# Kernel tuning notes

Hardware: AMD Instinct MI355X
Metric: run time of the kernel (lower is better)

Reference implementation:

```python
import jax, jax.numpy as jnp
import numpy as np

ALPHA = 0.25
GAMMA = 2.0
EPS = 1e-8
W_CLASS = 2.0
W_BBOX = 5.0
W_GIOU = 2.0
B, Q, T, C = 64, 900, 300, 80


def setup_inputs() -> dict:
    key = jax.random.key(0)
    k1, k2, k3, k4 = jax.random.split(key, 4)
    pred_logits = jax.random.normal(k1, (B, Q, C), dtype=jnp.float32)
    pred_boxes = jax.random.uniform(k2, (B, Q, 4), dtype=jnp.float32)  # cxcywh in (0,1)
    tgt_labels = jax.random.randint(k3, (B, T), 0, C, dtype=jnp.int64)
    tgt_boxes = jax.random.uniform(k4, (B, T, 4), dtype=jnp.float32)
    return {"pred_logits": pred_logits, "pred_boxes": pred_boxes,
            "tgt_labels": tgt_labels, "tgt_boxes": tgt_boxes}


def box_cxcywh_to_xyxy(b):
    cx, cy, w, h = b[..., 0], b[..., 1], b[..., 2], b[..., 3]
    return jnp.stack([cx - 0.5 * w, cy - 0.5 * h, cx + 0.5 * w, cy + 0.5 * h], axis=-1)


def pairwise_giou(boxes1, boxes2):
    # boxes1: [B,Q,4] xyxy, boxes2: [B,T,4] xyxy -> [B,Q,T]
    area1 = (boxes1[..., 2] - boxes1[..., 0]) * (boxes1[..., 3] - boxes1[..., 1])
    area2 = (boxes2[..., 2] - boxes2[..., 0]) * (boxes2[..., 3] - boxes2[..., 1])
    lt = jnp.maximum(boxes1[:, :, None, :2], boxes2[:, None, :, :2])
    rb = jnp.minimum(boxes1[:, :, None, 2:], boxes2[:, None, :, 2:])
    wh = jnp.clip(rb - lt, 0.0)
    inter = wh[..., 0] * wh[..., 1]
    union = area1[:, :, None] + area2[:, None, :] - inter
    iou = inter / union
    lt_c = jnp.minimum(boxes1[:, :, None, :2], boxes2[:, None, :, :2])
    rb_c = jnp.maximum(boxes1[:, :, None, 2:], boxes2[:, None, :, 2:])
    wh_c = jnp.clip(rb_c - lt_c, 0.0)
    area_c = wh_c[..., 0] * wh_c[..., 1]
    return iou - (area_c - union) / area_c


def reference(pred_logits, pred_boxes, tgt_labels, tgt_boxes):
    # Batched cost matrix of HungarianMatcher (use_focal_loss=True).
    prob = jax.nn.sigmoid(pred_logits)  # [B,Q,C]
    idx = jnp.broadcast_to(tgt_labels[:, None, :], (prob.shape[0], prob.shape[1], tgt_labels.shape[1]))
    p = jnp.take_along_axis(prob, idx.astype(jnp.int32), axis=2)  # [B,Q,T]
    neg_cost = (1.0 - ALPHA) * p ** GAMMA * (-jnp.log(1.0 - p + EPS))
    pos_cost = ALPHA * (1.0 - p) ** GAMMA * (-jnp.log(p + EPS))
    cost_class = pos_cost - neg_cost
    cost_bbox = jnp.abs(pred_boxes[:, :, None, :] - tgt_boxes[:, None, :, :]).sum(-1)
    cost_giou = -pairwise_giou(box_cxcywh_to_xyxy(pred_boxes), box_cxcywh_to_xyxy(tgt_boxes))
    cost = W_BBOX * cost_bbox + W_CLASS * cost_class + W_GIOU * cost_giou
    return jnp.nan_to_num(cost, nan=1.0, posinf=1e6, neginf=-1e6)
```

## Files before the change

kernel.cpp:

```cpp
#include <hip/hip_runtime.h>


constexpr int B = 64, Q = 900, T = 300, C = 80;
constexpr int QTILE = 25;
constexpr int BLOCK = 320;
constexpr float ALPHA = 0.25f;
constexpr float EPSF  = 1e-8f;

__device__ __forceinline__ float fast_rcp(float x) {
    return __builtin_amdgcn_rcpf(x);
}

__global__ __launch_bounds__(BLOCK) void matcher_cost_kernel(
    const float* __restrict__ logits,
    const float* __restrict__ pboxes,
    const int*   __restrict__ tlabels,
    const float* __restrict__ tboxes,
    float* __restrict__ out)
{
    __shared__ float  s_cls[QTILE * C];
    __shared__ float4 s_pA[QTILE];
    __shared__ float4 s_pB[QTILE];

    const int bid = blockIdx.x;
    const int b   = bid / (Q / QTILE);
    const int q0  = (bid % (Q / QTILE)) * QTILE;
    const int tid = threadIdx.x;

    float tcx = 0.f, tcy = 0.f, tw = 0.f, th = 0.f;
    float tx0 = 0.f, ty0 = 0.f, tx1 = 0.f, ty1 = 0.f, ta = 0.f;
    int lab = 0;
    if (tid < T) {
        float4 bx = *(const float4*)(tboxes + ((size_t)b * T + tid) * 4);
        tcx = bx.x; tcy = bx.y; tw = bx.z; th = bx.w;
        tx0 = bx.x - 0.5f * bx.z; ty0 = bx.y - 0.5f * bx.w;
        tx1 = bx.x + 0.5f * bx.z; ty1 = bx.y + 0.5f * bx.w;
        ta  = bx.z * bx.w;
        lab = tlabels[(size_t)b * T + tid];
    }

    if (tid < QTILE) {
        float4 bx = *(const float4*)(pboxes + ((size_t)b * Q + q0 + tid) * 4);
        float x0 = bx.x - 0.5f * bx.z, y0 = bx.y - 0.5f * bx.w;
        float x1 = bx.x + 0.5f * bx.z, y1 = bx.y + 0.5f * bx.w;
        s_pA[tid] = bx;
        s_pB[tid] = make_float4(x0, y0, x1, y1);
    }

    {
        const float* lg = logits + ((size_t)b * Q + q0) * C;
        for (int i = tid; i < QTILE * C; i += BLOCK) {
            float x  = lg[i];
            float pr = fast_rcp(1.0f + __expf(-x));
            float om = 1.0f - pr;
            float pos = ALPHA * om * om * (-__logf(pr + EPSF));
            float neg = (1.0f - ALPHA) * pr * pr * (-__logf(om + EPSF));
            s_cls[i] = 2.0f * (pos - neg) + 2.0f;
        }
    }

    __syncthreads();

    if (tid >= T) return;

    const float* clscol = s_cls + lab;
    float* op = out + ((size_t)b * Q + q0) * T + tid;
    #pragma unroll 5
    for (int ql = 0; ql < QTILE; ++ql) {
        float4 pA = s_pA[ql];
        float4 pB = s_pB[ql];
        float  pa = pA.z * pA.w;
        float clsv = clscol[ql * C];

        float cbbox = fabsf(pA.x - tcx) + fabsf(pA.y - tcy) +
                      fabsf(pA.z - tw ) + fabsf(pA.w - th );

        float iw = fmaxf(fminf(pB.z, tx1) - fmaxf(pB.x, tx0), 0.0f);
        float ih = fmaxf(fminf(pB.w, ty1) - fmaxf(pB.y, ty0), 0.0f);
        float inter = iw * ih;
        float uni   = pa + ta - inter;

        float cw = fmaxf(pB.z, tx1) - fminf(pB.x, tx0);
        float ch = fmaxf(pB.w, ty1) - fminf(pB.y, ty0);
        float ca = cw * ch;

        float c = fmaf(5.0f, cbbox, clsv);
        c = fmaf(-2.0f * inter, fast_rcp(uni), c);
        c = fmaf(-2.0f * uni,   fast_rcp(ca),  c);

        if (c != c) c = 1.0f;

        op[(size_t)ql * T] = c;
    }
}

extern "C" void kernel_launch(void* const* d_in, const int* in_sizes, int n_in,
                              void* d_out, int out_size, void* d_ws, size_t ws_size,
                              hipStream_t stream) {
    const float* logits  = (const float*)d_in[0];
    const float* pboxes  = (const float*)d_in[1];
    const int*   tlabels = (const int*)  d_in[2];
    const float* tboxes  = (const float*)d_in[3];
    float* out = (float*)d_out;

    dim3 grid(B * (Q / QTILE));
    dim3 block(BLOCK);
    matcher_cost_kernel<<<grid, block, 0, stream>>>(logits, pboxes, tlabels, tboxes, out);
}
```

Measured before the change: 38.21 us.

## Shrink Q tile, read pred boxes directly from global, preload class costs

Reduces the Q tile from 25 to 20 so the logits loop divides evenly by the block size and can be fully unrolled. Prediction boxes are no longer staged in shared memory. Each thread now loads them as uniform float4s from global memory and recomputes the xyxy corners itself. The per-thread class costs are gathered from shared memory into a register array up front, and the main loop is fully unrolled. This trades shared-memory staging and a sync dependency for more registers, redundant corner math, and more blocks with less work each.

Measured after the change: 37.28 us. -2.4%, faster.

```diff
diff --git a/kernel.cpp b/kernel.cpp
--- a/kernel.cpp
+++ b/kernel.cpp
@@ -2,7 +2,7 @@
 
 
 constexpr int B = 64, Q = 900, T = 300, C = 80;
-constexpr int QTILE = 25;
+constexpr int QTILE = 20;
 constexpr int BLOCK = 320;
 constexpr float ALPHA = 0.25f;
 constexpr float EPSF  = 1e-8f;
@@ -18,9 +18,7 @@
     const float* __restrict__ tboxes,
     float* __restrict__ out)
 {
-    __shared__ float  s_cls[QTILE * C];
-    __shared__ float4 s_pA[QTILE];
-    __shared__ float4 s_pB[QTILE];
+    __shared__ float s_cls[QTILE * C];
 
     const int bid = blockIdx.x;
     const int b   = bid / (Q / QTILE);
@@ -39,17 +37,11 @@
         lab = tlabels[(size_t)b * T + tid];
     }
 
-    if (tid < QTILE) {
-        float4 bx = *(const float4*)(pboxes + ((size_t)b * Q + q0 + tid) * 4);
-        float x0 = bx.x - 0.5f * bx.z, y0 = bx.y - 0.5f * bx.w;
-        float x1 = bx.x + 0.5f * bx.z, y1 = bx.y + 0.5f * bx.w;
-        s_pA[tid] = bx;
-        s_pB[tid] = make_float4(x0, y0, x1, y1);
-    }
-
     {
         const float* lg = logits + ((size_t)b * Q + q0) * C;
-        for (int i = tid; i < QTILE * C; i += BLOCK) {
+        #pragma unroll
+        for (int s = 0; s < QTILE * C / BLOCK; ++s) {
+            int i = s * BLOCK + tid;
             float x  = lg[i];
             float pr = fast_rcp(1.0f + __expf(-x));
             float om = 1.0f - pr;
@@ -63,28 +55,37 @@
 
     if (tid >= T) return;
 
-    const float* clscol = s_cls + lab;
+    float clsr[QTILE];
+    {
+        const float* cp = s_cls + lab;
+        #pragma unroll
+        for (int ql = 0; ql < QTILE; ++ql)
+            clsr[ql] = cp[ql * C];
+    }
+
+    const float4* pb = (const float4*)(pboxes + ((size_t)b * Q + q0) * 4);
     float* op = out + ((size_t)b * Q + q0) * T + tid;
-    #pragma unroll 5
+
+    #pragma unroll
     for (int ql = 0; ql < QTILE; ++ql) {
-        float4 pA = s_pA[ql];
-        float4 pB = s_pB[ql];
-        float  pa = pA.z * pA.w;
-        float clsv = clscol[ql * C];
+        float4 pA = pb[ql];
+        float px0 = pA.x - 0.5f * pA.z, py0 = pA.y - 0.5f * pA.w;
+        float px1 = pA.x + 0.5f * pA.z, py1 = pA.y + 0.5f * pA.w;
+        float pa  = pA.z * pA.w;
 
         float cbbox = fabsf(pA.x - tcx) + fabsf(pA.y - tcy) +
                       fabsf(pA.z - tw ) + fabsf(pA.w - th );
 
-        float iw = fmaxf(fminf(pB.z, tx1) - fmaxf(pB.x, tx0), 0.0f);
-        float ih = fmaxf(fminf(pB.w, ty1) - fmaxf(pB.y, ty0), 0.0f);
+        float iw = fmaxf(fminf(px1, tx1) - fmaxf(px0, tx0), 0.0f);
+        float ih = fmaxf(fminf(py1, ty1) - fmaxf(py0, ty0), 0.0f);
         float inter = iw * ih;
         float uni   = pa + ta - inter;
 
-        float cw = fmaxf(pB.z, tx1) - fminf(pB.x, tx0);
-        float ch = fmaxf(pB.w, ty1) - fminf(pB.y, ty0);
+        float cw = fmaxf(px1, tx1) - fminf(px0, tx0);
+        float ch = fmaxf(py1, ty1) - fminf(py0, ty0);
         float ca = cw * ch;
 
-        float c = fmaf(5.0f, cbbox, clsv);
+        float c = fmaf(5.0f, cbbox, clsr[ql]);
         c = fmaf(-2.0f * inter, fast_rcp(uni), c);
         c = fmaf(-2.0f * uni,   fast_rcp(ca),  c);
 
```

## Vectorize cost stores with per-thread 4-target float4 outputs and merged GIoU reciprocal

Applied to the files above, without the earlier changes.

Each thread now computes four consecutive targets for a strided set of queries and writes them as one float4 store. Target box data is staged in shared memory in SoA form so it can be read as float4. The two reciprocals in the GIoU term are merged into a single reciprocal of uni*ca, and the enclosing box width is derived algebraically from the intersection width. QTILE shrinks to 20 so the logits loop divides evenly, and launch bounds request 8 blocks per SM. The intent is fewer, wider global stores and fewer transcendental ops. The trade-off is more shared memory, scattered per-label shared reads, and a combined product that can overflow or lose precision differently from the reference.

Result: slower. 70.12 us (+83.5%).

```diff
diff --git a/kernel.cpp b/kernel.cpp
--- a/kernel.cpp
+++ b/kernel.cpp
@@ -2,8 +2,9 @@
 
 
 constexpr int B = 64, Q = 900, T = 300, C = 80;
-constexpr int QTILE = 25;
+constexpr int QTILE = 20;
 constexpr int BLOCK = 320;
+constexpr int NQ    = QTILE / 4;
 constexpr float ALPHA = 0.25f;
 constexpr float EPSF  = 1e-8f;
 
@@ -11,13 +12,23 @@
     return __builtin_amdgcn_rcpf(x);
 }
 
-__global__ __launch_bounds__(BLOCK) void matcher_cost_kernel(
+__device__ __forceinline__ float focal2(float x) {
+    float pr = fast_rcp(1.0f + __expf(-x));
+    float om = 1.0f - pr;
+    float pos = ALPHA * om * om * (-__logf(pr + EPSF));
+    float neg = (1.0f - ALPHA) * pr * pr * (-__logf(om + EPSF));
+    return 2.0f * (pos - neg) + 2.0f;
+}
+
+__global__ __launch_bounds__(BLOCK, 8) void matcher_cost_kernel(
     const float* __restrict__ logits,
     const float* __restrict__ pboxes,
     const int*   __restrict__ tlabels,
     const float* __restrict__ tboxes,
     float* __restrict__ out)
 {
+    __shared__ float4 s_t[8][T / 4];
+    __shared__ int4   s_tl[T / 4];
     __shared__ float  s_cls[QTILE * C];
     __shared__ float4 s_pA[QTILE];
     __shared__ float4 s_pB[QTILE];
@@ -27,70 +38,90 @@
     const int q0  = (bid % (Q / QTILE)) * QTILE;
     const int tid = threadIdx.x;
 
-    float tcx = 0.f, tcy = 0.f, tw = 0.f, th = 0.f;
-    float tx0 = 0.f, ty0 = 0.f, tx1 = 0.f, ty1 = 0.f, ta = 0.f;
-    int lab = 0;
     if (tid < T) {
         float4 bx = *(const float4*)(tboxes + ((size_t)b * T + tid) * 4);
-        tcx = bx.x; tcy = bx.y; tw = bx.z; th = bx.w;
-        tx0 = bx.x - 0.5f * bx.z; ty0 = bx.y - 0.5f * bx.w;
-        tx1 = bx.x + 0.5f * bx.z; ty1 = bx.y + 0.5f * bx.w;
-        ta  = bx.z * bx.w;
-        lab = tlabels[(size_t)b * T + tid];
+        float x0 = bx.x - 0.5f * bx.z, y0 = bx.y - 0.5f * bx.w;
+        float x1 = bx.x + 0.5f * bx.z, y1 = bx.y + 0.5f * bx.w;
+        ((float*)&s_t[0][0])[tid] = bx.x;
+        ((float*)&s_t[1][0])[tid] = bx.y;
+        ((float*)&s_t[2][0])[tid] = bx.z;
+        ((float*)&s_t[3][0])[tid] = bx.w;
+        ((float*)&s_t[4][0])[tid] = x0;
+        ((float*)&s_t[5][0])[tid] = y0;
+        ((float*)&s_t[6][0])[tid] = x1;
+        ((float*)&s_t[7][0])[tid] = y1;
+        ((int*)&s_tl[0])[tid]     = tlabels[(size_t)b * T + tid];
     }
-
     if (tid < QTILE) {
         float4 bx = *(const float4*)(pboxes + ((size_t)b * Q + q0 + tid) * 4);
-        float x0 = bx.x - 0.5f * bx.z, y0 = bx.y - 0.5f * bx.w;
-        float x1 = bx.x + 0.5f * bx.z, y1 = bx.y + 0.5f * bx.w;
         s_pA[tid] = bx;
-        s_pB[tid] = make_float4(x0, y0, x1, y1);
+        s_pB[tid] = make_float4(bx.x - 0.5f * bx.z, bx.y - 0.5f * bx.w,
+                                bx.x + 0.5f * bx.z, bx.y + 0.5f * bx.w);
     }
-
     {
         const float* lg = logits + ((size_t)b * Q + q0) * C;
-        for (int i = tid; i < QTILE * C; i += BLOCK) {
-            float x  = lg[i];
-            float pr = fast_rcp(1.0f + __expf(-x));
-            float om = 1.0f - pr;
-            float pos = ALPHA * om * om * (-__logf(pr + EPSF));
-            float neg = (1.0f - ALPHA) * pr * pr * (-__logf(om + EPSF));
-            s_cls[i] = 2.0f * (pos - neg) + 2.0f;
-        }
+        #pragma unroll
+        for (int s = 0; s < QTILE * C / BLOCK; ++s)
+            s_cls[s * BLOCK + tid] = focal2(lg[s * BLOCK + tid]);
     }
 
     __syncthreads();
 
     if (tid >= T) return;
 
-    const float* clscol = s_cls + lab;
-    float* op = out + ((size_t)b * Q + q0) * T + tid;
-    #pragma unroll 5
-    for (int ql = 0; ql < QTILE; ++ql) {
+    const int tq = tid / 75;
+    const int tt = tid - tq * 75;
+
+    float4 Tcx = s_t[0][tt], Tcy = s_t[1][tt];
+    float4 Tw  = s_t[2][tt], Th  = s_t[3][tt];
+    float4 Tx0 = s_t[4][tt], Ty0 = s_t[5][tt];
+    float4 Tx1 = s_t[6][tt], Ty1 = s_t[7][tt];
+    int4   lab = s_tl[tt];
+
+    const float* cls0 = s_cls + tq * C;
+    float* op = out + ((size_t)b * Q + q0 + tq) * T + tt * 4;
+
+    #pragma unroll
+    for (int j = 0; j < NQ; ++j) {
+        const int ql = tq + 4 * j;
         float4 pA = s_pA[ql];
         float4 pB = s_pB[ql];
         float  pa = pA.z * pA.w;
-        float clsv = clscol[ql * C];
+        const float* clsj = cls0 + j * 4 * C;
 
-        float cbbox = fabsf(pA.x - tcx) + fabsf(pA.y - tcy) +
-                      fabsf(pA.z - tw ) + fabsf(pA.w - th );
+        float cls_k[4] = { clsj[lab.x], clsj[lab.y], clsj[lab.z], clsj[lab.w] };
 
-        float iw = fmaxf(fminf(pB.z, tx1) - fmaxf(pB.x, tx0), 0.0f);
-        float ih = fmaxf(fminf(pB.w, ty1) - fmaxf(pB.y, ty0), 0.0f);
-        float inter = iw * ih;
-        float uni   = pa + ta - inter;
+        float4 res;
+        #pragma unroll
+        for (int k = 0; k < 4; ++k) {
+            float tcx_ = (&Tcx.x)[k], tcy_ = (&Tcy.x)[k];
+            float tw_  = (&Tw.x)[k],  th_  = (&Th.x)[k];
+            float tx0_ = (&Tx0.x)[k], ty0_ = (&Ty0.x)[k];
+            float tx1_ = (&Tx1.x)[k], ty1_ = (&Ty1.x)[k];
 
-        float cw = fmaxf(pB.z, tx1) - fminf(pB.x, tx0);
-        float ch = fmaxf(pB.w, ty1) - fminf(pB.y, ty0);
-        float ca = cw * ch;
+            float wi = fminf(pB.z, tx1_) - fmaxf(pB.x, tx0_);
+            float hi = fminf(pB.w, ty1_) - fmaxf(pB.y, ty0_);
+            float iw = fmaxf(wi, 0.0f), ih = fmaxf(hi, 0.0f);
+            float inter = iw * ih;
+            float ta  = tw_ * th_;
+            float uni = (pa + ta) - inter;
+            float cw  = (pA.z + tw_) - wi;
+            float ch  = (pA.w + th_) - hi;
+            float ca  = cw * ch;
 
-        float c = fmaf(5.0f, cbbox, clsv);
-        c = fmaf(-2.0f * inter, fast_rcp(uni), c);
-        c = fmaf(-2.0f * uni,   fast_rcp(ca),  c);
+            float cbbox = (fabsf(pA.x - tcx_) + fabsf(pA.y - tcy_)) +
+                          (fabsf(pA.z - tw_ ) + fabsf(pA.w - th_ ));
 
-        if (c != c) c = 1.0f;
+            float num = fmaf(uni, uni, inter * ca);
+            float r   = fast_rcp(uni * ca);
+            float c   = fmaf(5.0f, cbbox, cls_k[k]);
+            c = fmaf(num * r, -2.0f, c);
 
-        op[(size_t)ql * T] = c;
+            if (c != c) c = 1.0f;
+
+            (&res.x)[k] = c;
+        }
+        *(float4*)(op + (size_t)(4 * j) * T) = res;
     }
 }
 
```
